# Kernel optimization log

Hardware: AMD Instinct MI355X
Metric: run time of the kernel (lower is better)

## Reference

```python
import jax, jax.numpy as jnp
import numpy as np

HUMAN_EXHALATION_FLOW = 0.0052  # ENV_CONFIG.HUMAN_EXHALATION_FLOW
TIME_STEP = 1.0                 # ENV_CONFIG.TIME_STEP
N_NODES = 100_000
N_EDGES = 3_200_000
IN_DIM, OUT_DIM, K = 4, 1, 3
T_HIST = 16


def setup_inputs() -> dict:
    key = jax.random.key(0)
    k1, k2, k3, k4, k5 = jax.random.split(key, 5)
    # columns at [:, -1, :]: 0=concentration, 1=people, 2=size (size divides -> keep away from 0)
    origin_data = jax.random.uniform(k1, (N_NODES, T_HIST, 3), jnp.float32, 0.5, 1.5)
    # raw flow field: conv with kernel K (VALID) maps [E+K-1, K, IN_DIM] -> [E, 1, OUT_DIM]
    flow = jax.random.normal(k2, (N_EDGES + K - 1, K, IN_DIM), jnp.float32)
    edge_index = jax.random.randint(k3, (2, N_EDGES), 0, N_NODES, jnp.int32)
    conv_w = jax.random.normal(k4, (OUT_DIM, IN_DIM, K, K), jnp.float32) * 0.1
    conv_b = jax.random.normal(k5, (OUT_DIM,), jnp.float32) * 0.1
    return {"origin_data": origin_data, "flow": flow, "conv_w": conv_w,
            "conv_b": conv_b, "edge_index": edge_index}


def _flow_conv(flow, conv_w, conv_b):
    # [H, W, C] -> [1, C, H, W] -> conv -> [H', W', out_dim]
    x = jnp.transpose(flow, (2, 0, 1))[None]
    y = jax.lax.conv_general_dilated(
        x, conv_w, window_strides=(1, 1), padding='VALID',
        dimension_numbers=('NCHW', 'OIHW', 'NCHW'))
    y = y + conv_b[None, :, None, None]
    return jnp.transpose(y[0], (1, 2, 0))  # [E, 1, out_dim]


def reference(origin_data, flow, conv_w, conv_b, edge_index):
    concentration = origin_data[:, -1, 0]  # [N]
    people = origin_data[:, -1, 1]         # [N]
    size = origin_data[:, -1, 2]           # [N]
    n = concentration.shape[0]
    mask = jnp.ones((n,), concentration.dtype).at[-1].set(0.0)

    fc = _flow_conv(flow, conv_w, conv_b)  # [E, 1, 1]
    val = fc[:, 0, 0]                      # [E]

    src, dst = edge_index[0], edge_index[1]
    # original loop uses .item() everywhere -> these terms are detached from autodiff
    c_sg = jax.lax.stop_gradient(concentration)
    s_sg = jax.lax.stop_gradient(size)
    v_sg = jax.lax.stop_gradient(val)
    msg = jnp.where(src != dst, v_sg * c_sg[src], 0.0)  # skip self-loops
    node_new = jnp.zeros((n,), concentration.dtype)
    node_new = node_new.at[src].add(-msg / s_sg[src] * TIME_STEP)
    node_new = node_new.at[dst].add(msg / s_sg[dst] * TIME_STEP)

    exhaled = HUMAN_EXHALATION_FLOW * jax.lax.stop_gradient(people) / s_sg  # .item() loop -> detached
    result = concentration + (node_new + exhaled * TIME_STEP) * mask
    out2 = jnp.concatenate([edge_index.T.astype(val.dtype), fc[:, :, 0]], axis=1)  # [E, 3]
    return result[:, None], out2
```

## Files before the change

### kernel.cpp

```cpp
#include <hip/hip_runtime.h>


#define WSH    14
#define WSZ    16384
#define SLC    32
#define EPT    4
#define MAXWIN 16
#define OVSLOT 32

#define OWSH 13
#define OWSZ 8192
#define OPB  16
#define OFPS 8192.0f
#define OQBIAS (1 << 20)
#define OQCLMP ((1 << 19) - 1)

__global__ __launch_bounds__(256) void prep(
    const float* __restrict__ od,
    float* __restrict__ conc,
    unsigned long long* __restrict__ acc,
    unsigned* __restrict__ tails,
    int n_nodes)
{
    if (blockIdx.x == 0 && tails && threadIdx.x <= OVSLOT)
        tails[(size_t)threadIdx.x << 4] = 0u;
    int n = blockIdx.x * blockDim.x + threadIdx.x;
    if (n >= n_nodes) return;
    conc[n] = od[(long long)n * 48 + 45];
    if (acc) acc[n] = 0ULL;
}

__global__ __launch_bounds__(256) void edge_scatter(
    const float* __restrict__ flow, const int* __restrict__ ei,
    const float* __restrict__ conv_w, const float* __restrict__ conv_b,
    const float* __restrict__ conc,
    float* __restrict__ out2,
    uint2* __restrict__ rec,
    uint2* __restrict__ ovf,
    unsigned* __restrict__ tails,
    int n_edges, int n_win, unsigned cap, unsigned ocap)
{
    __shared__ float    w[40];
    __shared__ unsigned cnt[2 * MAXWIN];
    __shared__ unsigned sst[2 * MAXWIN];
    __shared__ unsigned bas[2 * MAXWIN];
    __shared__ unsigned stot;
    __shared__ uint2    stg[512 * EPT];
    __shared__ unsigned dsti[512 * EPT];

    const int t  = threadIdx.x;
    const int NB = 2 * n_win;
    if (t < 36) {
        int i  = t & 3;
        int kw = (t >> 2) % 3;
        int kh = t / 12;
        w[t] = conv_w[i * 9 + kh * 3 + kw];
    }
    if (t == 36) w[36] = conv_b[0];
    if (t < 2 * MAXWIN) cnt[t] = 0u;
    __syncthreads();

    const long long eb = (long long)blockIdx.x * (256 * EPT) + t;
    uint2    payA[EPT], payB[EPT];
    unsigned posA[EPT], posB[EPT];

#pragma unroll
    for (int k = 0; k < EPT; ++k) {
        posA[k] = 0xffffffffu; posB[k] = 0xffffffffu;
        long long e = eb + (long long)k * 256;
        if (e < n_edges) {
            int s = ei[e];
            int d = ei[n_edges + e];
            const float4* fp = (const float4*)(flow + e * 12);
            float acc = w[36];
#pragma unroll
            for (int q = 0; q < 9; ++q) {
                float4 v = fp[q];
                acc = fmaf(v.x, w[q * 4 + 0], acc);
                acc = fmaf(v.y, w[q * 4 + 1], acc);
                acc = fmaf(v.z, w[q * 4 + 2], acc);
                acc = fmaf(v.w, w[q * 4 + 3], acc);
            }
            float cs = conc[s];
            float* o = out2 + e * 3;
            o[0] = (float)s;
            o[1] = (float)d;
            o[2] = acc;
            if (s != d) {
                payA[k].x = (unsigned)s; payA[k].y = __float_as_uint(acc);
                payB[k].x = (unsigned)d; payB[k].y = __float_as_uint(acc * cs);
                posA[k] = atomicAdd(&cnt[(unsigned)s >> WSH], 1u);
                posB[k] = atomicAdd(&cnt[n_win + ((unsigned)d >> WSH)], 1u);
            }
        }
    }
    __syncthreads();

    if (t == 0) {
        unsigned a = 0;
        for (int b = 0; b < NB; ++b) { sst[b] = a; a += cnt[b]; }
        stot = a;
    }
    if (t < NB && cnt[t]) bas[t] = atomicAdd(&tails[(size_t)t << 4], cnt[t]);
    __syncthreads();

#pragma unroll
    for (int k = 0; k < EPT; ++k) {
        if (posA[k] != 0xffffffffu) {
            unsigned b = payA[k].x >> WSH;
            unsigned i = sst[b] + posA[k];
            unsigned g = bas[b] + posA[k];
            stg[i] = payA[k];
            if (g < cap) {
                dsti[i] = b * cap + g;
            } else {
                dsti[i] = 0xffffffffu;
                unsigned os = atomicAdd(&tails[(size_t)OVSLOT << 4], 1u);
                if (os < ocap) ovf[os] = payA[k];
            }
        }
        if (posB[k] != 0xffffffffu) {
            unsigned b = n_win + (payB[k].x >> WSH);
            unsigned i = sst[b] + posB[k];
            unsigned g = bas[b] + posB[k];
            stg[i] = payB[k];
            if (g < cap) {
                dsti[i] = b * cap + g;
            } else {
                dsti[i] = 0xffffffffu;
                unsigned os = atomicAdd(&tails[(size_t)OVSLOT << 4], 1u);
                if (os < ocap) { uint2 r = payB[k]; r.x |= 0x80000000u; ovf[os] = r; }
            }
        }
    }
    __syncthreads();

    unsigned tot = stot;
    for (unsigned i = t; i < tot; i += 256) {
        unsigned u = dsti[i];
        if (u != 0xffffffffu) rec[u] = stg[i];
    }
}

__global__ __launch_bounds__(1024) void accum_b(
    const uint2* __restrict__ rec, const uint2* __restrict__ ovf,
    const unsigned* __restrict__ tails,
    float* __restrict__ pA, float* __restrict__ pB,
    int n_win, unsigned cap, unsigned ocap)
{
    __shared__ float tA[WSZ];
    __shared__ float tB[WSZ];

    const int w  = blockIdx.x / SLC;
    const int sl = blockIdx.x % SLC;
    const int t  = threadIdx.x;

    float4 z = make_float4(0.f, 0.f, 0.f, 0.f);
    for (int i = t; i < (WSZ >> 2); i += 1024) {
        ((float4*)tA)[i] = z; ((float4*)tB)[i] = z;
    }
    __syncthreads();

    {
        unsigned nA = min(tails[(size_t)w << 4], cap);
        const uint2* r = rec + (size_t)w * cap;
        unsigned i0 = (unsigned)((unsigned long long)nA * sl / SLC);
        unsigned i1 = (unsigned)((unsigned long long)nA * (sl + 1) / SLC);
        for (unsigned i = i0 + t; i < i1; i += 1024) {
            uint2 q = r[i];
            atomicAdd(&tA[q.x & (WSZ - 1)], __uint_as_float(q.y));
        }
    }
    {
        unsigned nB = min(tails[(size_t)(n_win + w) << 4], cap);
        const uint2* r = rec + (size_t)(n_win + w) * cap;
        unsigned i0 = (unsigned)((unsigned long long)nB * sl / SLC);
        unsigned i1 = (unsigned)((unsigned long long)nB * (sl + 1) / SLC);
        for (unsigned i = i0 + t; i < i1; i += 1024) {
            uint2 q = r[i];
            atomicAdd(&tB[q.x & (WSZ - 1)], __uint_as_float(q.y));
        }
    }
    {
        unsigned no = min(tails[(size_t)OVSLOT << 4], ocap);
        if (no) {
            unsigned i0 = (unsigned)((unsigned long long)no * sl / SLC);
            unsigned i1 = (unsigned)((unsigned long long)no * (sl + 1) / SLC);
            for (unsigned i = i0 + t; i < i1; i += 1024) {
                uint2 q = ovf[i];
                unsigned node = q.x & 0x7fffffffu;
                if ((int)(node >> WSH) == w) {
                    if (q.x >> 31) atomicAdd(&tB[node & (WSZ - 1)], __uint_as_float(q.y));
                    else           atomicAdd(&tA[node & (WSZ - 1)], __uint_as_float(q.y));
                }
            }
        }
    }
    __syncthreads();

    float* dA = pA + ((size_t)blockIdx.x << WSH);
    float* dB = pB + ((size_t)blockIdx.x << WSH);
    for (int i = t; i < (WSZ >> 2); i += 1024) {
        ((float4*)dA)[i] = ((const float4*)tA)[i];
        ((float4*)dB)[i] = ((const float4*)tB)[i];
    }
}

__global__ __launch_bounds__(256) void node_final_b(
    const float* __restrict__ od,
    const float* __restrict__ conc,
    const float* __restrict__ pA,
    const float* __restrict__ pB,
    float* __restrict__ out, int n_nodes)
{
    int n = blockIdx.x * blockDim.x + threadIdx.x;
    if (n >= n_nodes) return;

    const int w = n >> WSH, i = n & (WSZ - 1);
    size_t base = ((size_t)(w * SLC) << WSH) + i;
    float a0 = 0.f, a1 = 0.f, b0 = 0.f, b1 = 0.f;
#pragma unroll
    for (int sl = 0; sl < SLC; sl += 2) {
        a0 += pA[base + ((size_t)(sl + 0) << WSH)];
        a1 += pA[base + ((size_t)(sl + 1) << WSH)];
        b0 += pB[base + ((size_t)(sl + 0) << WSH)];
        b1 += pB[base + ((size_t)(sl + 1) << WSH)];
    }
    float a = a0 + a1, b = b0 + b1;

    long long bi = (long long)n * 48 + 45;
    float c  = conc[n];
    float p  = od[bi + 1];
    float is = 1.0f / od[bi + 2];

    float r = c;
    if (n != n_nodes - 1)
        r += (b - a * c) * is + 0.0052f * p * is;
    out[n] = r;
}

__global__ __launch_bounds__(256) void edge_conv_o(
    const float* __restrict__ flow, const int* __restrict__ ei,
    const float* __restrict__ conv_w, const float* __restrict__ conv_b,
    float* __restrict__ out2, int n_edges)
{
    __shared__ float w[40];
    int t = threadIdx.x;
    if (t < 36) {
        int i  = t & 3;
        int kw = (t >> 2) % 3;
        int kh = t / 12;
        w[t] = conv_w[i * 9 + kh * 3 + kw];
    }
    if (t == 36) w[36] = conv_b[0];
    __syncthreads();

    int e = blockIdx.x * blockDim.x + t;
    if (e >= n_edges) return;

    const float4* fp = (const float4*)(flow + (long long)e * 12);
    float acc = w[36];
#pragma unroll
    for (int q = 0; q < 9; ++q) {
        float4 v = fp[q];
        acc = fmaf(v.x, w[q * 4 + 0], acc);
        acc = fmaf(v.y, w[q * 4 + 1], acc);
        acc = fmaf(v.z, w[q * 4 + 2], acc);
        acc = fmaf(v.w, w[q * 4 + 3], acc);
    }

    float* o = out2 + (long long)e * 3;
    o[0] = (float)ei[e];
    o[1] = (float)ei[n_edges + e];
    o[2] = acc;
}

__global__ __launch_bounds__(1024) void accum_o(
    const float* __restrict__ out2,
    const float* __restrict__ conc,
    unsigned long long* __restrict__ acc,
    int n_edges, int n_nodes)
{
    __shared__ float tA[OWSZ];
    __shared__ float tB[OWSZ];

    const int w    = blockIdx.x / OPB;
    const int sl   = blockIdx.x % OPB;
    const int base = w << OWSH;

    for (int i = threadIdx.x; i < OWSZ; i += 1024) { tA[i] = 0.f; tB[i] = 0.f; }
    __syncthreads();

    const long long e0 = (long long)sl * n_edges / OPB;
    const long long e1 = (long long)(sl + 1) * n_edges / OPB;
    for (long long e = e0 + threadIdx.x; e < e1; e += 1024) {
        const float* r = out2 + e * 3;
        float fs = r[0], fd = r[1], v = r[2];
        int s = (int)fs, d = (int)fd;
        if (s == d) continue;
        if ((s >> OWSH) == w) atomicAdd(&tA[s - base], v);
        if ((d >> OWSH) == w) atomicAdd(&tB[d - base], v * conc[s]);
    }
    __syncthreads();

    for (int i = threadIdx.x; i < OWSZ; i += 1024) {
        int n = base + i;
        if (n >= n_nodes) continue;
        float a = tA[i], b = tB[i];
        if (a == 0.f && b == 0.f) continue;
        int qa = __float2int_rn(a * OFPS);
        int qb = __float2int_rn(b * OFPS);
        qa = min(max(qa, -OQCLMP), OQCLMP);
        qb = min(max(qb, -OQCLMP), OQCLMP);
        unsigned long long enc =
            ((unsigned long long)(unsigned)(qa + OQBIAS) << 37) +
            ((unsigned long long)(unsigned)(qb + OQBIAS) << 10) + 1ULL;
        atomicAdd(acc + n, enc);
    }
}

__global__ __launch_bounds__(256) void node_final_o(
    const float* __restrict__ od,
    const float* __restrict__ conc,
    const unsigned long long* __restrict__ acc,
    float* __restrict__ out, int n_nodes)
{
    int n = blockIdx.x * blockDim.x + threadIdx.x;
    if (n >= n_nodes) return;

    unsigned long long t = acc[n];
    long long cnt = (long long)(t & 1023ULL);
    unsigned long long t2 = t >> 10;
    long long sbr = (long long)(t2 & ((1ULL << 27) - 1));
    long long sar = (long long)(t2 >> 27);
    float a = (float)(sar - cnt * OQBIAS) * (1.0f / OFPS);
    float b = (float)(sbr - cnt * OQBIAS) * (1.0f / OFPS);

    long long bi = (long long)n * 48 + 45;
    float c  = conc[n];
    float p  = od[bi + 1];
    float is = 1.0f / od[bi + 2];

    float r = c;
    if (n != n_nodes - 1)
        r += (b - a * c) * is + 0.0052f * p * is;
    out[n] = r;
}

extern "C" void kernel_launch(void* const* d_in, const int* in_sizes, int n_in,
                              void* d_out, int out_size, void* d_ws, size_t ws_size,
                              hipStream_t stream) {
    const float* od   = (const float*)d_in[0];
    const float* flow = (const float*)d_in[1];
    const float* cw   = (const float*)d_in[2];
    const float* cb   = (const float*)d_in[3];
    const int*   ei   = (const int*)d_in[4];

    const int n_nodes = in_sizes[0] / 48;
    const int n_edges = in_sizes[4] / 2;

    float* out_res = (float*)d_out;
    float* out2    = out_res + n_nodes;

    dim3 blk(256);
    dim3 grid_nodes((n_nodes + 255) / 256);

    const int n_win = (n_nodes + WSZ - 1) >> WSH;
    const int NB    = 2 * n_win;
    const unsigned cap  = (unsigned)(n_edges / (n_win > 0 ? n_win : 1))
                        + (unsigned)(n_edges / 8) + 4096u;
    const unsigned ocap = (unsigned)(2ULL * (unsigned long long)n_edges);

    size_t off = 0;
    size_t o_conc  = off; off += (((size_t)n_nodes * 4) + 255) & ~255ULL;
    size_t o_tails = off; off += ((OVSLOT + 1) * 16 * 4 + 255) & ~255ULL;
    size_t o_rec   = off; off += (((size_t)NB * cap * 8) + 255) & ~255ULL;
    size_t o_ovf   = off; off += (((size_t)ocap * 8) + 255) & ~255ULL;
    size_t o_pA    = off; off += (((size_t)n_win * SLC * WSZ * 4) + 255) & ~255ULL;
    size_t o_pB    = off; off += (((size_t)n_win * SLC * WSZ * 4) + 255) & ~255ULL;
    const bool full = (ws_size >= off) && (n_win <= MAXWIN);

    float* conc = (float*)((char*)d_ws + o_conc);

    if (full) {
        unsigned* tails = (unsigned*)((char*)d_ws + o_tails);
        uint2* rec = (uint2*)((char*)d_ws + o_rec);
        uint2* ovf = (uint2*)((char*)d_ws + o_ovf);
        float* pA  = (float*)((char*)d_ws + o_pA);
        float* pB  = (float*)((char*)d_ws + o_pB);

        dim3 grid_es((n_edges + 256 * EPT - 1) / (256 * EPT));

        prep<<<grid_nodes, blk, 0, stream>>>(od, conc, nullptr, tails, n_nodes);
        edge_scatter<<<grid_es, blk, 0, stream>>>(flow, ei, cw, cb, conc,
                                                  out2, rec, ovf, tails,
                                                  n_edges, n_win, cap, ocap);
        accum_b<<<dim3(n_win * SLC), dim3(1024), 0, stream>>>(
            rec, ovf, tails, pA, pB, n_win, cap, ocap);
        node_final_b<<<grid_nodes, blk, 0, stream>>>(od, conc, pA, pB,
                                                     out_res, n_nodes);
    } else {
        unsigned long long* acc =
            (unsigned long long*)((char*)d_ws + (((size_t)n_nodes * 4 + 7) / 8 * 8));
        const int n_win_o = (n_nodes + OWSZ - 1) >> OWSH;
        dim3 grid_edges((n_edges + 255) / 256);

        prep<<<grid_nodes, blk, 0, stream>>>(od, conc, acc, nullptr, n_nodes);
        edge_conv_o<<<grid_edges, blk, 0, stream>>>(flow, ei, cw, cb, out2, n_edges);
        accum_o<<<dim3(n_win_o * OPB), dim3(1024), 0, stream>>>(
            out2, conc, acc, n_edges, n_nodes);
        node_final_o<<<grid_nodes, blk, 0, stream>>>(od, conc, acc,
                                                     out_res, n_nodes);
    }
}
```

Measured before the change: 344.1 us.

## Share overlapping flow rows across edges via LDS and coalesce out2 stores

The edge kernel used to re-read nine float4s per edge from overlapping flow windows. It now loads each flow row once per 256-edge chunk and scatters the three kernel-row partial dot products into LDS with shared-memory atomics, then sums them per edge. The out2 triples are staged in LDS and written back as coalesced float4 stores. The dsti index array is removed and the destination bucket is recomputed with a linear search over prefix offsets, which shrinks LDS use. In exchange it adds extra barriers per chunk, LDS float atomics, and a serial bucket search in the final scatter.

```diff
diff --git a/kernel.cpp b/kernel.cpp
--- a/kernel.cpp
+++ b/kernel.cpp
@@ -42,11 +42,13 @@
 {
     __shared__ float    w[40];
     __shared__ unsigned cnt[2 * MAXWIN];
-    __shared__ unsigned sst[2 * MAXWIN];
+    __shared__ unsigned sst[2 * MAXWIN + 1];
     __shared__ unsigned bas[2 * MAXWIN];
     __shared__ unsigned stot;
-    __shared__ uint2    stg[512 * EPT];
-    __shared__ unsigned dsti[512 * EPT];
+    __shared__ __align__(16) char smem[16384];
+    float* R   = (float*)smem;
+    float* O   = (float*)smem + 780;
+    uint2* stg = (uint2*)smem;
 
     const int t  = threadIdx.x;
     const int NB = 2 * n_win;
@@ -58,47 +60,75 @@
     }
     if (t == 36) w[36] = conv_b[0];
     if (t < 2 * MAXWIN) cnt[t] = 0u;
-    __syncthreads();
-
-    const long long eb = (long long)blockIdx.x * (256 * EPT) + t;
+    for (int i = t; i < 774; i += 256) R[i] = 0.f;
+    __syncthreads();
+
     uint2    payA[EPT], payB[EPT];
     unsigned posA[EPT], posB[EPT];
+#pragma unroll
+    for (int k = 0; k < EPT; ++k) { posA[k] = 0xffffffffu; posB[k] = 0xffffffffu; }
 
 #pragma unroll
     for (int k = 0; k < EPT; ++k) {
-        posA[k] = 0xffffffffu; posB[k] = 0xffffffffu;
-        long long e = eb + (long long)k * 256;
+        const long long E0 = (long long)blockIdx.x * (256 * EPT) + (long long)k * 256;
+        if (E0 >= n_edges) break;
+        const int nrows = (int)(((long long)n_edges + 2 - E0) < 258 ?
+                                ((long long)n_edges + 2 - E0) : 258);
+        const int nf4 = 3 * nrows;
+
+        const float4* fb = (const float4*)flow + E0 * 3;
+        for (int i = t; i < nf4; i += 256) {
+            float4 v = fb[i];
+            int row = i / 3;
+            int kk  = (i - row * 3) << 2;
+            float d0 = fmaf(v.x, w[kk +  0], fmaf(v.y, w[kk +  1],
+                       fmaf(v.z, w[kk +  2], v.w * w[kk +  3])));
+            float d1 = fmaf(v.x, w[kk + 12], fmaf(v.y, w[kk + 13],
+                       fmaf(v.z, w[kk + 14], v.w * w[kk + 15])));
+            float d2 = fmaf(v.x, w[kk + 24], fmaf(v.y, w[kk + 25],
+                       fmaf(v.z, w[kk + 26], v.w * w[kk + 27])));
+            atomicAdd(&R[row],       d0);
+            atomicAdd(&R[258 + row], d1);
+            atomicAdd(&R[516 + row], d2);
+        }
+        __syncthreads();
+
+        const long long e = E0 + t;
         if (e < n_edges) {
+            float val = w[36] + R[t] + R[258 + t + 1] + R[516 + t + 2];
             int s = ei[e];
             int d = ei[n_edges + e];
-            const float4* fp = (const float4*)(flow + e * 12);
-            float acc = w[36];
-#pragma unroll
-            for (int q = 0; q < 9; ++q) {
-                float4 v = fp[q];
-                acc = fmaf(v.x, w[q * 4 + 0], acc);
-                acc = fmaf(v.y, w[q * 4 + 1], acc);
-                acc = fmaf(v.z, w[q * 4 + 2], acc);
-                acc = fmaf(v.w, w[q * 4 + 3], acc);
-            }
             float cs = conc[s];
-            float* o = out2 + e * 3;
-            o[0] = (float)s;
-            o[1] = (float)d;
-            o[2] = acc;
+            O[t * 3 + 0] = (float)s;
+            O[t * 3 + 1] = (float)d;
+            O[t * 3 + 2] = val;
             if (s != d) {
-                payA[k].x = (unsigned)s; payA[k].y = __float_as_uint(acc);
-                payB[k].x = (unsigned)d; payB[k].y = __float_as_uint(acc * cs);
+                payA[k].x = (unsigned)s; payA[k].y = __float_as_uint(val);
+                payB[k].x = (unsigned)d; payB[k].y = __float_as_uint(val * cs);
                 posA[k] = atomicAdd(&cnt[(unsigned)s >> WSH], 1u);
                 posB[k] = atomicAdd(&cnt[n_win + ((unsigned)d >> WSH)], 1u);
             }
         }
-    }
-    __syncthreads();
+        __syncthreads();
+
+        {
+            long long fbase = E0 * 3;
+            long long nfl = ((long long)n_edges - E0) * 3;
+            if (nfl >= 768) {
+                if (t < 192) ((float4*)(out2 + fbase))[t] = ((const float4*)O)[t];
+            } else {
+                for (int i = t; i < (int)nfl; i += 256) out2[fbase + i] = O[i];
+            }
+            if (k + 1 < EPT)
+                for (int i = t; i < 774; i += 256) R[i] = 0.f;
+        }
+        __syncthreads();
+    }
 
     if (t == 0) {
         unsigned a = 0;
         for (int b = 0; b < NB; ++b) { sst[b] = a; a += cnt[b]; }
+        sst[NB] = a;
         stot = a;
     }
     if (t < NB && cnt[t]) bas[t] = atomicAdd(&tails[(size_t)t << 4], cnt[t]);
@@ -108,37 +138,30 @@
     for (int k = 0; k < EPT; ++k) {
         if (posA[k] != 0xffffffffu) {
             unsigned b = payA[k].x >> WSH;
-            unsigned i = sst[b] + posA[k];
-            unsigned g = bas[b] + posA[k];
-            stg[i] = payA[k];
-            if (g < cap) {
-                dsti[i] = b * cap + g;
-            } else {
-                dsti[i] = 0xffffffffu;
-                unsigned os = atomicAdd(&tails[(size_t)OVSLOT << 4], 1u);
-                if (os < ocap) ovf[os] = payA[k];
-            }
+            stg[sst[b] + posA[k]] = payA[k];
         }
         if (posB[k] != 0xffffffffu) {
             unsigned b = n_win + (payB[k].x >> WSH);
-            unsigned i = sst[b] + posB[k];
-            unsigned g = bas[b] + posB[k];
-            stg[i] = payB[k];
-            if (g < cap) {
-                dsti[i] = b * cap + g;
-            } else {
-                dsti[i] = 0xffffffffu;
-                unsigned os = atomicAdd(&tails[(size_t)OVSLOT << 4], 1u);
-                if (os < ocap) { uint2 r = payB[k]; r.x |= 0x80000000u; ovf[os] = r; }
+            stg[sst[b] + posB[k]] = payB[k];
+        }
+    }
+    __syncthreads();
+
+    const unsigned tot = stot;
+    for (unsigned i = t; i < tot; i += 256) {
+        unsigned b = 0;
+        while (i >= sst[b + 1]) ++b;
+        unsigned g = bas[b] + (i - sst[b]);
+        uint2 r = stg[i];
+        if (g < cap) {
+            rec[(size_t)b * cap + g] = r;
+        } else {
+            unsigned os = atomicAdd(&tails[(size_t)OVSLOT << 4], 1u);
+            if (os < ocap) {
+                if ((int)b >= n_win) r.x |= 0x80000000u;
+                ovf[os] = r;
             }
         }
-    }
-    __syncthreads();
-
-    unsigned tot = stot;
-    for (unsigned i = t; i < tot; i += 256) {
-        unsigned u = dsti[i];
-        if (u != 0xffffffffu) rec[u] = stg[i];
     }
 }
 
```

After: 467.8 us. 1.36x slower.
